# Kernel tuning notes

Hardware: AMD Instinct MI355X
Metric: run time of the kernel (lower is better)

## Reference

```python
import jax, jax.numpy as jnp
import numpy as np

B, T, D, H, L = 8, 150, 30, 5, 3
HD = D // H  # 6
ORIG = (300, 74, 35)


def setup_inputs() -> dict:
    key = jax.random.key(0)
    ks = iter(jax.random.split(key, 40))
    def g(shape, s=0.05):
        return jax.random.normal(next(ks), shape, dtype=jnp.float32) * s
    return {
        "x_l": g((B, T, ORIG[0]), 1.0),
        "x_a": g((B, T, ORIG[1]), 1.0),
        "x_v": g((B, T, ORIG[2]), 1.0),
        "Wl": g((D, ORIG[0])),
        "Wa": g((D, ORIG[1])),
        "Wv": g((D, ORIG[2])),
        "in_w": g((2, L, 3 * D, D)),
        "in_b": jnp.zeros((2, L, 3 * D), jnp.float32),
        "out_w": g((2, L, D, D)),
        "out_b": jnp.zeros((2, L, D), jnp.float32),
        "lin1_w": g((2, L, 4 * D, D)),
        "lin1_b": jnp.zeros((2, L, 4 * D), jnp.float32),
        "lin2_w": g((2, L, D, 4 * D)),
        "lin2_b": jnp.zeros((2, L, D), jnp.float32),
        "n1_g": jnp.ones((2, L, D), jnp.float32),
        "n1_b": jnp.zeros((2, L, D), jnp.float32),
        "n2_g": jnp.ones((2, L, D), jnp.float32),
        "n2_b": jnp.zeros((2, L, D), jnp.float32),
        "p1_w": g((2 * D, 2 * D)),
        "p1_b": jnp.zeros((2 * D,), jnp.float32),
        "p2_w": g((2 * D, 2 * D)),
        "p2_b": jnp.zeros((2 * D,), jnp.float32),
        "ow": g((1, 2 * D)),
        "ob": jnp.zeros((1,), jnp.float32),
    }


def _ln(x, g, b, eps=1e-5):
    m = x.mean(-1, keepdims=True)
    v = jnp.var(x, axis=-1, keepdims=True)  # biased var, matches torch LayerNorm
    return (x - m) * jax.lax.rsqrt(v + eps) * g + b


def _heads(x):  # [Tt, B, D] -> [B*H, Tt, HD]
    Tt = x.shape[0]
    return x.reshape(Tt, B * H, HD).transpose(1, 0, 2)


def _layer(x, xk, xv, p):
    iw, ib, ow, ob, w1, b1, w2, b2, g1, bb1, g2, bb2 = p
    res = x
    xn, kn, vn = _ln(x, g1, bb1), _ln(xk, g1, bb1), _ln(xv, g1, bb1)
    q = (xn @ iw[:D].T + ib[:D]) * (HD ** -0.5)
    k = kn @ iw[D:2 * D].T + ib[D:2 * D]
    v = vn @ iw[2 * D:].T + ib[2 * D:]
    qh, kh, vh = _heads(q), _heads(k), _heads(v)
    # trilinear scores: [B*H, Tq, Tk, Tv]
    aw = jnp.einsum('iat,ibt,ict->iabc', qh, kh, vh)
    fused = aw.mean(-1) + aw.max(-1)          # fuse over value axis -> [B*H, Tq, Tk]
    fused = jax.nn.softmax(fused, axis=-1)
    attn = jnp.einsum('iab,ibt->iat', fused, qh)  # NB: original bmm uses q, not v
    attn = attn.transpose(1, 0, 2).reshape(-1, B, D)
    x = res + (attn @ ow.T + ob)
    res = x
    xn = _ln(x, g2, bb2)
    x = jax.nn.relu(xn @ w1.T + b1) @ w2.T + b2
    return res + x


def reference(x_l, x_a, x_v, Wl, Wa, Wv, in_w, in_b, out_w, out_b,
              lin1_w, lin1_b, lin2_w, lin2_b, n1_g, n1_b, n2_g, n2_b,
              p1_w, p1_b, p2_w, p2_b, ow, ob):
    pl = (x_l @ Wl.T).transpose(1, 0, 2)  # [T, B, D] (conv1d k=1, no bias)
    pa = (x_a @ Wa.T).transpose(1, 0, 2)
    pv = (x_v @ Wv.T).transpose(1, 0, 2)
    hs = []
    for s, (kk, vv) in enumerate(((pa, pv), (pv, pa))):
        h = pl
        for l in range(L):
            p = (in_w[s, l], in_b[s, l], out_w[s, l], out_b[s, l],
                 lin1_w[s, l], lin1_b[s, l], lin2_w[s, l], lin2_b[s, l],
                 n1_g[s, l], n1_b[s, l], n2_g[s, l], n2_b[s, l])
            h = _layer(h, kk, vv, p)
        hs.append(h[-1])  # last timestep [B, D]
    last_hs = jnp.concatenate(hs, axis=1)  # [B, 2D]
    proj = jax.nn.relu(last_hs @ p1_w.T + p1_b) @ p2_w.T + p2_b + last_hs
    out = proj @ ow.T + ob
    return (out, last_hs)
```

## Files before the change

kernel.cpp:

```cpp
#include <hip/hip_runtime.h>
#include <math.h>

#define BB 8
#define TT 150
#define DD 30
#define HH 5
#define HD 6
#define LL 3
#define NI 40
#define ROWF (TT*BB*DD)
#define RSTR 8
#define NR 152

typedef _Float16 half8 __attribute__((ext_vector_type(8)));
typedef float f32x16 __attribute__((ext_vector_type(16)));

__device__ __forceinline__ float wsum(float v) {
    #pragma unroll
    for (int m = 32; m > 0; m >>= 1) v += __shfl_xor(v, m, 64);
    return v;
}

__global__ __launch_bounds__(256) void proj3_kernel(
    const float* __restrict__ x_l, const float* __restrict__ x_a, const float* __restrict__ x_v,
    const float* __restrict__ Wl, const float* __restrict__ Wa, const float* __restrict__ Wv,
    float* __restrict__ pl, float* __restrict__ pa, float* __restrict__ pv) {
    int blk = blockIdx.x;
    int which = blk / 300;
    int w = threadIdx.x >> 6, lane = threadIdx.x & 63;
    int rowu = (blk % 300) * 4 + w;
    int t = rowu / BB, b = rowu % BB;
    const float* x = which == 0 ? x_l : (which == 1 ? x_a : x_v);
    const float* W = which == 0 ? Wl : (which == 1 ? Wa : Wv);
    float* out = which == 0 ? pl : (which == 1 ? pa : pv);
    int Cin = which == 0 ? 300 : (which == 1 ? 74 : 35);
    int cst = Cin + ((Cin & 1) ? 0 : 1);
    __shared__ float WS[30 * 301];
    __shared__ float xr[4][304];
    for (int j = threadIdx.x; j < DD * Cin; j += 256)
        WS[(j / Cin) * cst + (j % Cin)] = W[j];
    const float* xp = x + ((size_t)b * TT + t) * Cin;
    for (int j = lane; j < Cin; j += 64) xr[w][j] = xp[j];
    __syncthreads();
    int d = lane >> 1, jh = lane & 1;
    int h1 = Cin >> 1;
    int j0 = jh ? h1 : 0, j1 = jh ? Cin : h1;
    const float* wr = WS + (size_t)(d < DD ? d : 0) * cst;
    float acc = 0.f;
    for (int j = j0; j < j1; j++) acc += xr[w][j] * wr[j];
    acc += __shfl_xor(acc, 1, 64);
    if (jh == 0 && d < DD) out[t * (BB * DD) + b * DD + d] = acc;
}

__global__ __launch_bounds__(256) void kvpre_kernel(
    const float* __restrict__ pa, const float* __restrict__ pv,
    const float* __restrict__ in_w, const float* __restrict__ in_b,
    const float* __restrict__ n1g, const float* __restrict__ n1b,
    float* __restrict__ k_all, float* __restrict__ v_all) {
    int blk = blockIdx.x;
    int po = blk / 300;
    int s = po / LL;
    int w = threadIdx.x >> 6, lane = threadIdx.x & 63;
    int tb = (blk % 300) * 4 + w;
    int t = tb / BB, b = tb % BB;
    const float* xk = (s == 0) ? pa : pv;
    const float* xv = (s == 0) ? pv : pa;
    const float* iw = in_w + (size_t)po * 2700 + 900;
    const float* ib = in_b + (size_t)po * 90;
    const float* g  = n1g + (size_t)po * 30;
    const float* bb = n1b + (size_t)po * 30;
    __shared__ float iwS[1800];
    __shared__ float xn[4][2][30];
    for (int j = threadIdx.x; j < 1800; j += 256) iwS[j] = iw[j];
    const float* rows[2] = { xk + (size_t)tb * 30, xv + (size_t)tb * 30 };
    for (int r = 0; r < 2; r++) {
        float xval = (lane < 30) ? rows[r][lane] : 0.f;
        float mean = wsum(xval) * (1.f / 30.f);
        float dv = (lane < 30) ? (xval - mean) : 0.f;
        float var = wsum(dv * dv) * (1.f / 30.f);
        float inv = rsqrtf(var + 1e-5f);
        if (lane < 30) xn[w][r][lane] = dv * inv * g[lane] + bb[lane];
    }
    __syncthreads();
    int o = lane;
    if (o < 60) {
        int which = o / 30, dd = o % 30;
        const float* wr = iwS + o * 30;
        const float* xr = xn[w][which];
        float acc = 0.f;
        #pragma unroll 6
        for (int j = 0; j < 30; j++) acc += wr[j] * xr[j];
        acc += ib[30 + o];
        int i = b * HH + dd / HD, hd = dd % HD;
        float* dst = which ? v_all : k_all;
        dst[((size_t)po * NI + i) * (TT * HD) + t * HD + hd] = acc;
    }
}

__global__ __launch_bounds__(256) void lnq0_kernel(
    const float* __restrict__ pl,
    const float* __restrict__ in_w, const float* __restrict__ in_b,
    const float* __restrict__ n1g, const float* __restrict__ n1b,
    float* __restrict__ q) {
    int blk = blockIdx.x;
    int s = blk / 300;
    int w = threadIdx.x >> 6, lane = threadIdx.x & 63;
    int tb = (blk % 300) * 4 + w;
    int t = tb / BB, b = tb % BB;
    int po = s * LL;
    const float* iw = in_w + (size_t)po * 2700;
    const float* ib = in_b + (size_t)po * 90;
    const float* g  = n1g + (size_t)po * 30;
    const float* bb = n1b + (size_t)po * 30;
    __shared__ float iwS[900];
    __shared__ float xn[4][30];
    for (int j = threadIdx.x; j < 900; j += 256) iwS[j] = iw[j];
    const float* row = pl + (size_t)tb * 30;
    float xval = (lane < 30) ? row[lane] : 0.f;
    float mean = wsum(xval) * (1.f / 30.f);
    float dv = (lane < 30) ? (xval - mean) : 0.f;
    float var = wsum(dv * dv) * (1.f / 30.f);
    float inv = rsqrtf(var + 1e-5f);
    if (lane < 30) xn[w][lane] = dv * inv * g[lane] + bb[lane];
    __syncthreads();
    int o = lane;
    if (o < 30) {
        const float* wr = iwS + o * 30;
        float acc = 0.f;
        #pragma unroll 6
        for (int j = 0; j < 30; j++) acc += wr[j] * xn[w][j];
        acc = (acc + ib[o]) * 0.40824829046386307f;
        int i = b * HH + o / HD, hd = o % HD;
        q[((size_t)s * NI + i) * (TT * HD) + t * HD + hd] = acc;
    }
}

__global__ __launch_bounds__(256) void score_kernel(
    const float* __restrict__ q, const float* __restrict__ k_all,
    const float* __restrict__ v_all, int l, float* __restrict__ attn) {
    int blk = blockIdx.x;
    int s = blk / 760;
    int rem = blk % 760;
    int i = rem / 19;
    int g = rem % 19;
    int tid = threadIdx.x;
    int wv = tid >> 6, lane = tid & 63;
    int lo = lane & 31, hf = lane >> 5;
    int po = s * LL + l;

    __shared__ __align__(16) _Float16 qsh[NR * RSTR];
    __shared__ __align__(16) _Float16 ksh[NR * RSTR];
    __shared__ __align__(16) _Float16 vsh[NR * RSTR];

    int* qz = (int*)qsh; int* kz = (int*)ksh; int* vz = (int*)vsh;
    for (int idx = tid; idx < NR * RSTR / 2; idx += 256) {
        qz[idx] = 0; kz[idx] = 0; vz[idx] = 0;
    }
    __syncthreads();
    const float* qg = q + (size_t)(s * NI + i) * (TT * HD);
    const float* kg = k_all + (size_t)(po * NI + i) * (TT * HD);
    const float* vg = v_all + (size_t)(po * NI + i) * (TT * HD);
    for (int idx = tid; idx < TT * HD; idx += 256) {
        int dst = (idx / HD) * RSTR + (idx % HD);
        qsh[dst] = (_Float16)qg[idx];
        ksh[dst] = (_Float16)kg[idx];
        vsh[dst] = (_Float16)vg[idx];
    }
    __syncthreads();
    if (wv == 0) {
        float v6[6] = {0.f, 0.f, 0.f, 0.f, 0.f, 0.f};
        for (int c = lane; c < TT; c += 64) {
            #pragma unroll
            for (int t = 0; t < 6; t++) v6[t] += (float)vsh[c * RSTR + t];
        }
        #pragma unroll
        for (int m = 32; m > 0; m >>= 1) {
            #pragma unroll
            for (int t = 0; t < 6; t++) v6[t] += __shfl_xor(v6[t], m, 64);
        }
        if (lane < 6) vsh[TT * RSTR + lane] = (_Float16)(v6[lane] * (1.f / TT));
    }
    __syncthreads();

    f32x16 zacc;
    #pragma unroll
    for (int j = 0; j < 16; j++) zacc[j] = 0.f;
    half8 zero8;
    #pragma unroll
    for (int t = 0; t < 8; t++) zero8[t] = (_Float16)0.f;

    half8 bfrag[5], vhalf[5];
    #pragma unroll
    for (int nt = 0; nt < 5; nt++) {
        int rr = nt * 32 + lo;
        int rc = rr < 151 ? rr : 151;
        half8 kf = *(const half8*)&ksh[rc * RSTR];
        half8 vf = *(const half8*)&vsh[rc * RSTR];
        bfrag[nt] = hf ? zero8 : kf;
        vhalf[nt] = hf ? zero8 : vf;
    }

    for (int ap = 0; ap < 2; ap++) {
        int a = g * 8 + wv * 2 + ap;
        if (a >= TT) break;
        half8 qav = *(const half8*)&qsh[a * RSTR];
        half8 afrag[5];
        #pragma unroll
        for (int nt = 0; nt < 5; nt++) afrag[nt] = vhalf[nt] * qav;

        float fsc[5];
        #pragma unroll
        for (int nb = 0; nb < 5; nb++) {
            float rm = -INFINITY;
            #pragma unroll
            for (int ma = 0; ma < 4; ma++) {
                f32x16 acc = __builtin_amdgcn_mfma_f32_32x32x16_f16(afrag[ma], bfrag[nb], zacc, 0, 0, 0);
                float m = fmaxf(acc[0], acc[1]);
                #pragma unroll
                for (int j = 2; j < 16; j += 2) m = fmaxf(fmaxf(m, acc[j]), acc[j + 1]);
                rm = fmaxf(rm, m);
            }
            f32x16 a4 = __builtin_amdgcn_mfma_f32_32x32x16_f16(afrag[4], bfrag[nb], zacc, 0, 0, 0);
            float m4 = fmaxf(a4[0], a4[1]);
            #pragma unroll
            for (int j = 2; j < 10; j += 2) m4 = fmaxf(fmaxf(m4, a4[j]), a4[j + 1]);
            float ext = (hf == 0) ? fmaxf(a4[10], a4[11]) : -INFINITY;
            rm = fmaxf(rm, fmaxf(m4, ext));
            float om = __shfl_xor(a4[10], 32, 64);
            float mn = hf ? a4[10] : om;
            rm = fmaxf(rm, __shfl_xor(rm, 32, 64));
            int bcol = nb * 32 + lo;
            fsc[nb] = (bcol < TT) ? (mn + rm) : -INFINITY;
        }
        float m = fsc[0];
        #pragma unroll
        for (int nb = 1; nb < 5; nb++) m = fmaxf(m, fsc[nb]);
        #pragma unroll
        for (int msk = 16; msk > 0; msk >>= 1) m = fmaxf(m, __shfl_xor(m, msk, 64));
        float e[5], es = 0.f;
        #pragma unroll
        for (int nb = 0; nb < 5; nb++) { e[nb] = __expf(fsc[nb] - m); es += e[nb]; }
        #pragma unroll
        for (int msk = 16; msk > 0; msk >>= 1) es += __shfl_xor(es, msk, 64);
        float acc6[6] = {0.f, 0.f, 0.f, 0.f, 0.f, 0.f};
        #pragma unroll
        for (int nb = 0; nb < 5; nb++) {
            int bcol = nb * 32 + lo;
            int bi = (bcol < TT) ? bcol : 0;
            float wgt = e[nb];
            half8 qrow = *(const half8*)&qsh[bi * RSTR];
            #pragma unroll
            for (int t = 0; t < 6; t++) acc6[t] += wgt * (float)qrow[t];
        }
        #pragma unroll
        for (int msk = 16; msk > 0; msk >>= 1) {
            #pragma unroll
            for (int t = 0; t < 6; t++) acc6[t] += __shfl_xor(acc6[t], msk, 64);
        }
        if (lane == 0) {
            float inv = 1.f / es;
            int bo = i / HH, ho = i % HH;
            float* dst = attn + (size_t)s * ROWF + a * (BB * DD) + bo * DD + ho * HD;
            #pragma unroll
            for (int t = 0; t < 6; t++) dst[t] = acc6[t] * inv;
        }
    }
}

__global__ __launch_bounds__(256) void ffnlnq_kernel(
    const float* __restrict__ attn, const float* __restrict__ pl,
    const float* __restrict__ out_w, const float* __restrict__ out_b,
    const float* __restrict__ l1w, const float* __restrict__ l1b,
    const float* __restrict__ l2w, const float* __restrict__ l2b,
    const float* __restrict__ n2g, const float* __restrict__ n2b,
    const float* __restrict__ in_w, const float* __restrict__ in_b,
    const float* __restrict__ n1g, const float* __restrict__ n1b,
    int l, int has_next,
    float* __restrict__ h, float* __restrict__ q) {
    int blk = blockIdx.x;
    int s = blk / 300;
    int w = threadIdx.x >> 6, lane = threadIdx.x & 63;
    int tb = (blk % 300) * 4 + w;
    int t = tb / BB, b = tb % BB;
    int po = s * LL + l;
    const float* ow = out_w + (size_t)po * 900;
    const float* ob = out_b + (size_t)po * 30;
    const float* w1 = l1w + (size_t)po * 3600;
    const float* b1 = l1b + (size_t)po * 120;
    const float* w2 = l2w + (size_t)po * 3600;
    const float* b2 = l2b + (size_t)po * 30;
    const float* g2 = n2g + (size_t)po * 30;
    const float* bb2 = n2b + (size_t)po * 30;
    __shared__ float owS[900];
    __shared__ float w1T[30 * 128];
    __shared__ float w2S[30 * 121];
    __shared__ float iwqS[900];
    __shared__ float arS[4][30], xnS[4][32], hidS[4][120], xqS[4][30];
    for (int j = threadIdx.x; j < 900; j += 256) owS[j] = ow[j];
    for (int j = threadIdx.x; j < 3600; j += 256) w1T[(j % 30) * 128 + (j / 30)] = w1[j];
    for (int j = threadIdx.x; j < 3600; j += 256) w2S[(j / 120) * 121 + (j % 120)] = w2[j];
    if (has_next) {
        const float* iwq = in_w + (size_t)(po + 1) * 2700;
        for (int j = threadIdx.x; j < 900; j += 256) iwqS[j] = iwq[j];
    }
    __syncthreads();
    float* hrow = h + (size_t)s * ROWF + (size_t)tb * 30;
    const float* res = (l == 0) ? (pl + (size_t)tb * 30) : hrow;
    const float* arow = attn + (size_t)s * ROWF + (size_t)tb * 30;
    if (lane < 30) arS[w][lane] = arow[lane];
    float x1v = 0.f;
    if (lane < 30) {
        const float* wr = owS + lane * 30;
        float acc = 0.f;
        #pragma unroll 6
        for (int j = 0; j < 30; j++) acc += wr[j] * arS[w][j];
        x1v = res[lane] + acc + ob[lane];
    }
    float mean = wsum(x1v) * (1.f / 30.f);
    float dv = (lane < 30) ? (x1v - mean) : 0.f;
    float var = wsum(dv * dv) * (1.f / 30.f);
    float inv = rsqrtf(var + 1e-5f);
    if (lane < 30) xnS[w][lane] = dv * inv * g2[lane] + bb2[lane];
    for (int o = lane; o < 120; o += 64) {
        float acc = 0.f;
        #pragma unroll 6
        for (int j = 0; j < 30; j++) acc += w1T[j * 128 + o] * xnS[w][j];
        hidS[w][o] = fmaxf(acc + b1[o], 0.f);
    }
    float newh = 0.f;
    if (lane < 30) {
        const float* wr = w2S + lane * 121;
        float acc = 0.f;
        #pragma unroll 8
        for (int j = 0; j < 120; j++) acc += wr[j] * hidS[w][j];
        newh = x1v + acc + b2[lane];
        hrow[lane] = newh;
    }
    if (has_next) {
        const float* g1 = n1g + (size_t)(po + 1) * 30;
        const float* bb1 = n1b + (size_t)(po + 1) * 30;
        const float* ibq = in_b + (size_t)(po + 1) * 90;
        float mean2 = wsum(newh) * (1.f / 30.f);
        float dv2 = (lane < 30) ? (newh - mean2) : 0.f;
        float var2 = wsum(dv2 * dv2) * (1.f / 30.f);
        float inv2 = rsqrtf(var2 + 1e-5f);
        if (lane < 30) xqS[w][lane] = dv2 * inv2 * g1[lane] + bb1[lane];
        int o = lane;
        if (o < 30) {
            const float* wr = iwqS + o * 30;
            float acc = 0.f;
            #pragma unroll 6
            for (int j = 0; j < 30; j++) acc += wr[j] * xqS[w][j];
            acc = (acc + ibq[o]) * 0.40824829046386307f;
            int i = b * HH + o / HD, hd = o % HD;
            q[((size_t)s * NI + i) * (TT * HD) + t * HD + hd] = acc;
        }
    }
}

__global__ __launch_bounds__(256) void head_kernel(
    const float* __restrict__ h,
    const float* __restrict__ p1w, const float* __restrict__ p1b,
    const float* __restrict__ p2w, const float* __restrict__ p2b,
    const float* __restrict__ ow, const float* __restrict__ ob,
    float* __restrict__ out) {
    int tid = threadIdx.x;
    __shared__ float lh[480], hid[480], pr[480];
    for (int idx = tid; idx < 480; idx += 256) {
        int b = idx / 60, j = idx % 60;
        int s = j / 30, d = j % 30;
        float vv = h[(size_t)s * ROWF + 149 * (BB * DD) + b * DD + d];
        lh[idx] = vv;
        out[8 + idx] = vv;
    }
    __syncthreads();
    for (int idx = tid; idx < 480; idx += 256) {
        int b = idx / 60, o = idx % 60;
        const float* wr = p1w + o * 60;
        float acc = p1b[o];
        for (int j = 0; j < 60; j++) acc += wr[j] * lh[b * 60 + j];
        hid[idx] = fmaxf(acc, 0.f);
    }
    __syncthreads();
    for (int idx = tid; idx < 480; idx += 256) {
        int b = idx / 60, d = idx % 60;
        const float* wr = p2w + d * 60;
        float acc = p2b[d];
        for (int j = 0; j < 60; j++) acc += wr[j] * hid[b * 60 + j];
        pr[idx] = acc + lh[idx];
    }
    __syncthreads();
    if (tid < 8) {
        float acc = ob[0];
        for (int j = 0; j < 60; j++) acc += pr[tid * 60 + j] * ow[j];
        out[tid] = acc;
    }
}

extern "C" void kernel_launch(void* const* d_in, const int* in_sizes, int n_in,
                              void* d_out, int out_size, void* d_ws, size_t ws_size,
                              hipStream_t stream) {
    const float* x_l   = (const float*)d_in[0];
    const float* x_a   = (const float*)d_in[1];
    const float* x_v   = (const float*)d_in[2];
    const float* Wl    = (const float*)d_in[3];
    const float* Wa    = (const float*)d_in[4];
    const float* Wv    = (const float*)d_in[5];
    const float* in_w  = (const float*)d_in[6];
    const float* in_b  = (const float*)d_in[7];
    const float* out_w = (const float*)d_in[8];
    const float* out_b = (const float*)d_in[9];
    const float* l1w   = (const float*)d_in[10];
    const float* l1b   = (const float*)d_in[11];
    const float* l2w   = (const float*)d_in[12];
    const float* l2b   = (const float*)d_in[13];
    const float* n1g   = (const float*)d_in[14];
    const float* n1b   = (const float*)d_in[15];
    const float* n2g   = (const float*)d_in[16];
    const float* n2b   = (const float*)d_in[17];
    const float* p1w   = (const float*)d_in[18];
    const float* p1b   = (const float*)d_in[19];
    const float* p2w   = (const float*)d_in[20];
    const float* p2b   = (const float*)d_in[21];
    const float* oww   = (const float*)d_in[22];
    const float* obb   = (const float*)d_in[23];

    float* ws = (float*)d_ws;
    float* pl    = ws;
    float* pa    = ws + 36000;
    float* pv    = ws + 72000;
    float* h     = ws + 108000;
    float* q     = ws + 180000;
    float* k_all = ws + 252000;
    float* v_all = ws + 468000;
    float* at    = ws + 684000;

    proj3_kernel<<<900, 256, 0, stream>>>(x_l, x_a, x_v, Wl, Wa, Wv, pl, pa, pv);
    kvpre_kernel<<<1800, 256, 0, stream>>>(pa, pv, in_w, in_b, n1g, n1b, k_all, v_all);
    lnq0_kernel<<<600, 256, 0, stream>>>(pl, in_w, in_b, n1g, n1b, q);

    for (int l = 0; l < LL; l++) {
        score_kernel<<<1520, 256, 0, stream>>>(q, k_all, v_all, l, at);
        ffnlnq_kernel<<<600, 256, 0, stream>>>(at, pl, out_w, out_b, l1w, l1b, l2w, l2b,
                                               n2g, n2b, in_w, in_b, n1g, n1b,
                                               l, (l < LL - 1) ? 1 : 0, h, q);
    }
    head_kernel<<<1, 256, 0, stream>>>(h, p1w, p1b, p2w, p2b, oww, obb, (float*)d_out);
}
```

Before: 254.2 us.

## Fuse all stages into one cooperative persistent kernel with grid syncs

Replaces the ten separate kernel launches with a single cooperative persistent kernel. Blocks loop over tasks for each stage and use grid.sync between stages, which removes launch gaps and per-launch overhead. The input-projection weights are now staged in shared memory as fp16. The grid is capped at 768 blocks with two blocks per CU, so each block handles several tasks per stage serially and grid-wide barriers are added. The old multi-kernel path stays as a fallback.

```diff
diff --git a/kernel.cpp b/kernel.cpp
--- a/kernel.cpp
+++ b/kernel.cpp
@@ -1,5 +1,8 @@
 #include <hip/hip_runtime.h>
+#include <hip/hip_cooperative_groups.h>
 #include <math.h>
+
+namespace cg = cooperative_groups;
 
 #define BB 8
 #define TT 150
@@ -11,14 +14,390 @@
 #define ROWF (TT*BB*DD)
 #define RSTR 8
 #define NR 152
+#define SMEMN 9904
 
 typedef _Float16 half8 __attribute__((ext_vector_type(8)));
 typedef float f32x16 __attribute__((ext_vector_type(16)));
+
+struct Params {
+    const float *x_l, *x_a, *x_v, *Wl, *Wa, *Wv;
+    const float *in_w, *in_b, *out_w, *out_b;
+    const float *l1w, *l1b, *l2w, *l2b;
+    const float *n1g, *n1b, *n2g, *n2b;
+    const float *p1w, *p1b, *p2w, *p2b, *oww, *obb;
+    float *pl, *pa, *pv, *h, *q, *k_all, *v_all, *at, *out;
+};
 
 __device__ __forceinline__ float wsum(float v) {
     #pragma unroll
     for (int m = 32; m > 0; m >>= 1) v += __shfl_xor(v, m, 64);
     return v;
+}
+
+__global__ __launch_bounds__(256, 2) void mega_kernel(Params P) {
+    cg::grid_group grid = cg::this_grid();
+    __shared__ __align__(16) float sm[SMEMN];
+    const int tid = threadIdx.x;
+    const int w = tid >> 6, lane = tid & 63;
+    const int nbk = gridDim.x, bid = blockIdx.x;
+
+    {
+        _Float16* WH = (_Float16*)sm;
+        float* xr = sm + 4520;
+        for (int task = bid; task < 900; task += nbk) {
+            int which = task / 300;
+            int rowu = (task % 300) * 4 + w;
+            int t = rowu / BB, b = rowu % BB;
+            const float* x = which == 0 ? P.x_l : (which == 1 ? P.x_a : P.x_v);
+            const float* W = which == 0 ? P.Wl : (which == 1 ? P.Wa : P.Wv);
+            float* outp = which == 0 ? P.pl : (which == 1 ? P.pa : P.pv);
+            int Cin = which == 0 ? 300 : (which == 1 ? 74 : 35);
+            int cst = Cin | 1;
+            for (int j = tid; j < DD * Cin; j += 256)
+                WH[(j / Cin) * cst + (j % Cin)] = (_Float16)W[j];
+            const float* xp = x + ((size_t)b * TT + t) * Cin;
+            for (int j = lane; j < Cin; j += 64) xr[w * 304 + j] = xp[j];
+            __syncthreads();
+            int d = lane >> 1, jh = lane & 1;
+            int h1 = Cin >> 1;
+            int j0 = jh ? h1 : 0, j1 = jh ? Cin : h1;
+            const _Float16* wr = WH + (d < DD ? d : 0) * cst;
+            float acc = 0.f;
+            for (int j = j0; j < j1; j++) acc += xr[w * 304 + j] * (float)wr[j];
+            acc += __shfl_xor(acc, 1, 64);
+            if (jh == 0 && d < DD) outp[t * (BB * DD) + b * DD + d] = acc;
+            __syncthreads();
+        }
+    }
+    __threadfence();
+    grid.sync();
+
+    {
+        float* iwS = sm;
+        float* xn  = sm + 1800;
+        for (int task = bid; task < 1800; task += nbk) {
+            int po = task / 300;
+            int s = po / LL;
+            int tb = (task % 300) * 4 + w;
+            int t = tb / BB, b = tb % BB;
+            const float* xk = (s == 0) ? P.pa : P.pv;
+            const float* xv = (s == 0) ? P.pv : P.pa;
+            const float* iw = P.in_w + (size_t)po * 2700 + 900;
+            const float* ib = P.in_b + (size_t)po * 90;
+            const float* g  = P.n1g + (size_t)po * 30;
+            const float* bb = P.n1b + (size_t)po * 30;
+            for (int j = tid; j < 1800; j += 256) iwS[j] = iw[j];
+            const float* rows[2] = { xk + (size_t)tb * 30, xv + (size_t)tb * 30 };
+            for (int r = 0; r < 2; r++) {
+                float xval = (lane < 30) ? rows[r][lane] : 0.f;
+                float mean = wsum(xval) * (1.f / 30.f);
+                float dv = (lane < 30) ? (xval - mean) : 0.f;
+                float var = wsum(dv * dv) * (1.f / 30.f);
+                float inv = rsqrtf(var + 1e-5f);
+                if (lane < 30) xn[w * 60 + r * 30 + lane] = dv * inv * g[lane] + bb[lane];
+            }
+            __syncthreads();
+            if (lane < 60) {
+                int which = lane / 30, dd = lane % 30;
+                const float* wr = iwS + lane * 30;
+                const float* xv2 = xn + w * 60 + which * 30;
+                float acc = 0.f;
+                #pragma unroll 6
+                for (int j = 0; j < 30; j++) acc += wr[j] * xv2[j];
+                acc += ib[30 + lane];
+                int i = b * HH + dd / HD, hd = dd % HD;
+                float* dst = which ? P.v_all : P.k_all;
+                dst[((size_t)po * NI + i) * (TT * HD) + t * HD + hd] = acc;
+            }
+            __syncthreads();
+        }
+        float* iwq = sm;
+        float* xn2 = sm + 900;
+        for (int task = bid; task < 600; task += nbk) {
+            int s = task / 300;
+            int tb = (task % 300) * 4 + w;
+            int t = tb / BB, b = tb % BB;
+            int po = s * LL;
+            const float* iw = P.in_w + (size_t)po * 2700;
+            const float* ib = P.in_b + (size_t)po * 90;
+            const float* g  = P.n1g + (size_t)po * 30;
+            const float* bb = P.n1b + (size_t)po * 30;
+            for (int j = tid; j < 900; j += 256) iwq[j] = iw[j];
+            const float* row = P.pl + (size_t)tb * 30;
+            float xval = (lane < 30) ? row[lane] : 0.f;
+            float mean = wsum(xval) * (1.f / 30.f);
+            float dv = (lane < 30) ? (xval - mean) : 0.f;
+            float var = wsum(dv * dv) * (1.f / 30.f);
+            float inv = rsqrtf(var + 1e-5f);
+            if (lane < 30) xn2[w * 30 + lane] = dv * inv * g[lane] + bb[lane];
+            __syncthreads();
+            if (lane < 30) {
+                const float* wr = iwq + lane * 30;
+                float acc = 0.f;
+                #pragma unroll 6
+                for (int j = 0; j < 30; j++) acc += wr[j] * xn2[w * 30 + j];
+                acc = (acc + ib[lane]) * 0.40824829046386307f;
+                int i = b * HH + lane / HD, hd = lane % HD;
+                P.q[((size_t)s * NI + i) * (TT * HD) + t * HD + hd] = acc;
+            }
+            __syncthreads();
+        }
+    }
+    __threadfence();
+    grid.sync();
+
+    for (int l = 0; l < LL; l++) {
+        {
+            _Float16* qsh = (_Float16*)sm;
+            _Float16* ksh = qsh + NR * RSTR;
+            _Float16* vsh = ksh + NR * RSTR;
+            const int lo = lane & 31, hf = lane >> 5;
+            for (int task = bid; task < 1520; task += nbk) {
+                int s = task / 760;
+                int rem = task % 760;
+                int i = rem / 19;
+                int g = rem % 19;
+                int po = s * LL + l;
+                int* z = (int*)sm;
+                for (int idx = tid; idx < 3 * NR * RSTR / 2; idx += 256) z[idx] = 0;
+                __syncthreads();
+                const float* qg = P.q + (size_t)(s * NI + i) * (TT * HD);
+                const float* kg = P.k_all + (size_t)(po * NI + i) * (TT * HD);
+                const float* vg = P.v_all + (size_t)(po * NI + i) * (TT * HD);
+                for (int idx = tid; idx < TT * HD; idx += 256) {
+                    int dst = (idx / HD) * RSTR + (idx % HD);
+                    qsh[dst] = (_Float16)qg[idx];
+                    ksh[dst] = (_Float16)kg[idx];
+                    vsh[dst] = (_Float16)vg[idx];
+                }
+                __syncthreads();
+                if (w == 0) {
+                    float v6[6] = {0.f, 0.f, 0.f, 0.f, 0.f, 0.f};
+                    for (int c = lane; c < TT; c += 64) {
+                        #pragma unroll
+                        for (int t = 0; t < 6; t++) v6[t] += (float)vsh[c * RSTR + t];
+                    }
+                    #pragma unroll
+                    for (int m = 32; m > 0; m >>= 1) {
+                        #pragma unroll
+                        for (int t = 0; t < 6; t++) v6[t] += __shfl_xor(v6[t], m, 64);
+                    }
+                    if (lane < 6) vsh[TT * RSTR + lane] = (_Float16)(v6[lane] * (1.f / TT));
+                }
+                __syncthreads();
+
+                f32x16 zacc;
+                #pragma unroll
+                for (int j = 0; j < 16; j++) zacc[j] = 0.f;
+                half8 zero8;
+                #pragma unroll
+                for (int t = 0; t < 8; t++) zero8[t] = (_Float16)0.f;
+
+                half8 bfrag[5], vhalf[5];
+                #pragma unroll
+                for (int nt = 0; nt < 5; nt++) {
+                    int rr = nt * 32 + lo;
+                    int rc = rr < 151 ? rr : 151;
+                    half8 kf = *(const half8*)&ksh[rc * RSTR];
+                    half8 vf = *(const half8*)&vsh[rc * RSTR];
+                    bfrag[nt] = hf ? zero8 : kf;
+                    vhalf[nt] = hf ? zero8 : vf;
+                }
+
+                for (int ap = 0; ap < 2; ap++) {
+                    int a = g * 8 + w * 2 + ap;
+                    if (a >= TT) break;
+                    half8 qav = *(const half8*)&qsh[a * RSTR];
+                    half8 afrag[5];
+                    #pragma unroll
+                    for (int nt = 0; nt < 5; nt++) afrag[nt] = vhalf[nt] * qav;
+
+                    float fsc[5];
+                    #pragma unroll
+                    for (int nb = 0; nb < 5; nb++) {
+                        float rm = -INFINITY;
+                        #pragma unroll
+                        for (int ma = 0; ma < 4; ma++) {
+                            f32x16 acc = __builtin_amdgcn_mfma_f32_32x32x16_f16(afrag[ma], bfrag[nb], zacc, 0, 0, 0);
+                            float m = fmaxf(acc[0], acc[1]);
+                            #pragma unroll
+                            for (int j = 2; j < 16; j += 2) m = fmaxf(fmaxf(m, acc[j]), acc[j + 1]);
+                            rm = fmaxf(rm, m);
+                        }
+                        f32x16 a4 = __builtin_amdgcn_mfma_f32_32x32x16_f16(afrag[4], bfrag[nb], zacc, 0, 0, 0);
+                        float m4 = fmaxf(a4[0], a4[1]);
+                        #pragma unroll
+                        for (int j = 2; j < 10; j += 2) m4 = fmaxf(fmaxf(m4, a4[j]), a4[j + 1]);
+                        float ext = (hf == 0) ? fmaxf(a4[10], a4[11]) : -INFINITY;
+                        rm = fmaxf(rm, fmaxf(m4, ext));
+                        float om = __shfl_xor(a4[10], 32, 64);
+                        float mn = hf ? a4[10] : om;
+                        rm = fmaxf(rm, __shfl_xor(rm, 32, 64));
+                        int bcol = nb * 32 + lo;
+                        fsc[nb] = (bcol < TT) ? (mn + rm) : -INFINITY;
+                    }
+                    float m = fsc[0];
+                    #pragma unroll
+                    for (int nb = 1; nb < 5; nb++) m = fmaxf(m, fsc[nb]);
+                    #pragma unroll
+                    for (int msk = 16; msk > 0; msk >>= 1) m = fmaxf(m, __shfl_xor(m, msk, 64));
+                    float e[5], es = 0.f;
+                    #pragma unroll
+                    for (int nb = 0; nb < 5; nb++) { e[nb] = __expf(fsc[nb] - m); es += e[nb]; }
+                    #pragma unroll
+                    for (int msk = 16; msk > 0; msk >>= 1) es += __shfl_xor(es, msk, 64);
+                    float acc6[6] = {0.f, 0.f, 0.f, 0.f, 0.f, 0.f};
+                    #pragma unroll
+                    for (int nb = 0; nb < 5; nb++) {
+                        int bcol = nb * 32 + lo;
+                        int bi = (bcol < TT) ? bcol : 0;
+                        float wgt = e[nb];
+                        half8 qrow = *(const half8*)&qsh[bi * RSTR];
+                        #pragma unroll
+                        for (int t = 0; t < 6; t++) acc6[t] += wgt * (float)qrow[t];
+                    }
+                    #pragma unroll
+                    for (int msk = 16; msk > 0; msk >>= 1) {
+                        #pragma unroll
+                        for (int t = 0; t < 6; t++) acc6[t] += __shfl_xor(acc6[t], msk, 64);
+                    }
+                    if (lane == 0) {
+                        float inv = 1.f / es;
+                        int bo = i / HH, ho = i % HH;
+                        float* dst = P.at + (size_t)s * ROWF + a * (BB * DD) + bo * DD + ho * HD;
+                        #pragma unroll
+                        for (int t = 0; t < 6; t++) dst[t] = acc6[t] * inv;
+                    }
+                }
+                __syncthreads();
+            }
+        }
+        __threadfence();
+        grid.sync();
+
+        {
+            float* owS  = sm;
+            float* w1T  = sm + 900;
+            float* w2S  = sm + 4500;
+            float* iwqS = sm + 8130;
+            float* arS  = sm + 9030;
+            float* xnS  = sm + 9150;
+            float* hidS = sm + 9278;
+            float* xqS  = sm + 9758;
+            int has_next = (l < LL - 1);
+            for (int task = bid; task < 600; task += nbk) {
+                int s = task / 300;
+                int tb = (task % 300) * 4 + w;
+                int t = tb / BB, b = tb % BB;
+                int po = s * LL + l;
+                const float* ow = P.out_w + (size_t)po * 900;
+                const float* ob = P.out_b + (size_t)po * 30;
+                const float* w1 = P.l1w + (size_t)po * 3600;
+                const float* b1 = P.l1b + (size_t)po * 120;
+                const float* w2 = P.l2w + (size_t)po * 3600;
+                const float* b2 = P.l2b + (size_t)po * 30;
+                const float* g2 = P.n2g + (size_t)po * 30;
+                const float* bb2 = P.n2b + (size_t)po * 30;
+                for (int j = tid; j < 900; j += 256) owS[j] = ow[j];
+                for (int j = tid; j < 3600; j += 256) w1T[(j % 30) * 120 + (j / 30)] = w1[j];
+                for (int j = tid; j < 3600; j += 256) w2S[(j / 120) * 121 + (j % 120)] = w2[j];
+                if (has_next) {
+                    const float* iwq = P.in_w + (size_t)(po + 1) * 2700;
+                    for (int j = tid; j < 900; j += 256) iwqS[j] = iwq[j];
+                }
+                float* hrow = P.h + (size_t)s * ROWF + (size_t)tb * 30;
+                const float* res = (l == 0) ? (P.pl + (size_t)tb * 30) : hrow;
+                const float* arow = P.at + (size_t)s * ROWF + (size_t)tb * 30;
+                if (lane < 30) arS[w * 30 + lane] = arow[lane];
+                __syncthreads();
+                float x1v = 0.f;
+                if (lane < 30) {
+                    const float* wr = owS + lane * 30;
+                    float acc = 0.f;
+                    #pragma unroll 6
+                    for (int j = 0; j < 30; j++) acc += wr[j] * arS[w * 30 + j];
+                    x1v = res[lane] + acc + ob[lane];
+                }
+                float mean = wsum(x1v) * (1.f / 30.f);
+                float dv = (lane < 30) ? (x1v - mean) : 0.f;
+                float var = wsum(dv * dv) * (1.f / 30.f);
+                float inv = rsqrtf(var + 1e-5f);
+                if (lane < 30) xnS[w * 32 + lane] = dv * inv * g2[lane] + bb2[lane];
+                for (int o = lane; o < 120; o += 64) {
+                    float acc = 0.f;
+                    #pragma unroll 6
+                    for (int j = 0; j < 30; j++) acc += w1T[j * 120 + o] * xnS[w * 32 + j];
+                    hidS[w * 120 + o] = fmaxf(acc + b1[o], 0.f);
+                }
+                float newh = 0.f;
+                if (lane < 30) {
+                    const float* wr = w2S + lane * 121;
+                    float acc = 0.f;
+                    #pragma unroll 8
+                    for (int j = 0; j < 120; j++) acc += wr[j] * hidS[w * 120 + j];
+                    newh = x1v + acc + b2[lane];
+                    hrow[lane] = newh;
+                }
+                if (has_next) {
+                    const float* g1 = P.n1g + (size_t)(po + 1) * 30;
+                    const float* bb1 = P.n1b + (size_t)(po + 1) * 30;
+                    const float* ibq = P.in_b + (size_t)(po + 1) * 90;
+                    float mean2 = wsum(newh) * (1.f / 30.f);
+                    float dv2 = (lane < 30) ? (newh - mean2) : 0.f;
+                    float var2 = wsum(dv2 * dv2) * (1.f / 30.f);
+                    float inv2 = rsqrtf(var2 + 1e-5f);
+                    if (lane < 30) xqS[w * 30 + lane] = dv2 * inv2 * g1[lane] + bb1[lane];
+                    if (lane < 30) {
+                        const float* wr = iwqS + lane * 30;
+                        float acc = 0.f;
+                        #pragma unroll 6
+                        for (int j = 0; j < 30; j++) acc += wr[j] * xqS[w * 30 + j];
+                        acc = (acc + ibq[lane]) * 0.40824829046386307f;
+                        int i = b * HH + lane / HD, hd = lane % HD;
+                        P.q[((size_t)s * NI + i) * (TT * HD) + t * HD + hd] = acc;
+                    }
+                }
+                __syncthreads();
+            }
+        }
+        __threadfence();
+        grid.sync();
+    }
+
+    if (bid == 0) {
+        float* lh  = sm;
+        float* hid = sm + 480;
+        float* pr  = sm + 960;
+        for (int idx = tid; idx < 480; idx += 256) {
+            int b = idx / 60, j = idx % 60;
+            int s = j / 30, d = j % 30;
+            float vv = P.h[(size_t)s * ROWF + 149 * (BB * DD) + b * DD + d];
+            lh[idx] = vv;
+            P.out[8 + idx] = vv;
+        }
+        __syncthreads();
+        for (int idx = tid; idx < 480; idx += 256) {
+            int b = idx / 60, o = idx % 60;
+            const float* wr = P.p1w + o * 60;
+            float acc = P.p1b[o];
+            for (int j = 0; j < 60; j++) acc += wr[j] * lh[b * 60 + j];
+            hid[idx] = fmaxf(acc, 0.f);
+        }
+        __syncthreads();
+        for (int idx = tid; idx < 480; idx += 256) {
+            int b = idx / 60, d = idx % 60;
+            const float* wr = P.p2w + d * 60;
+            float acc = P.p2b[d];
+            for (int j = 0; j < 60; j++) acc += wr[j] * hid[b * 60 + j];
+            pr[idx] = acc + lh[idx];
+        }
+        __syncthreads();
+        if (tid < 8) {
+            float acc = P.obb[0];
+            for (int j = 0; j < 60; j++) acc += pr[tid * 60 + j] * P.oww[j];
+            P.out[tid] = acc;
+        }
+    }
 }
 
 __global__ __launch_bounds__(256) void proj3_kernel(
@@ -34,7 +413,7 @@
     const float* W = which == 0 ? Wl : (which == 1 ? Wa : Wv);
     float* out = which == 0 ? pl : (which == 1 ? pa : pv);
     int Cin = which == 0 ? 300 : (which == 1 ? 74 : 35);
-    int cst = Cin + ((Cin & 1) ? 0 : 1);
+    int cst = Cin | 1;
     __shared__ float WS[30 * 301];
     __shared__ float xr[4][304];
     for (int j = threadIdx.x; j < DD * Cin; j += 256)
@@ -82,15 +461,14 @@
         if (lane < 30) xn[w][r][lane] = dv * inv * g[lane] + bb[lane];
     }
     __syncthreads();
-    int o = lane;
-    if (o < 60) {
-        int which = o / 30, dd = o % 30;
-        const float* wr = iwS + o * 30;
-        const float* xr = xn[w][which];
+    if (lane < 60) {
+        int which = lane / 30, dd = lane % 30;
+        const float* wr = iwS + lane * 30;
+        const float* xv2 = xn[w][which];
         float acc = 0.f;
         #pragma unroll 6
-        for (int j = 0; j < 30; j++) acc += wr[j] * xr[j];
-        acc += ib[30 + o];
+        for (int j = 0; j < 30; j++) acc += wr[j] * xv2[j];
+        acc += ib[30 + lane];
         int i = b * HH + dd / HD, hd = dd % HD;
         float* dst = which ? v_all : k_all;
         dst[((size_t)po * NI + i) * (TT * HD) + t * HD + hd] = acc;
@@ -123,14 +501,13 @@
     float inv = rsqrtf(var + 1e-5f);
     if (lane < 30) xn[w][lane] = dv * inv * g[lane] + bb[lane];
     __syncthreads();
-    int o = lane;
-    if (o < 30) {
-        const float* wr = iwS + o * 30;
+    if (lane < 30) {
+        const float* wr = iwS + lane * 30;
         float acc = 0.f;
         #pragma unroll 6
         for (int j = 0; j < 30; j++) acc += wr[j] * xn[w][j];
-        acc = (acc + ib[o]) * 0.40824829046386307f;
-        int i = b * HH + o / HD, hd = o % HD;
+        acc = (acc + ib[lane]) * 0.40824829046386307f;
+        int i = b * HH + lane / HD, hd = lane % HD;
         q[((size_t)s * NI + i) * (TT * HD) + t * HD + hd] = acc;
     }
 }
@@ -147,15 +524,11 @@
     int wv = tid >> 6, lane = tid & 63;
     int lo = lane & 31, hf = lane >> 5;
     int po = s * LL + l;
-
     __shared__ __align__(16) _Float16 qsh[NR * RSTR];
     __shared__ __align__(16) _Float16 ksh[NR * RSTR];
     __shared__ __align__(16) _Float16 vsh[NR * RSTR];
-
     int* qz = (int*)qsh; int* kz = (int*)ksh; int* vz = (int*)vsh;
-    for (int idx = tid; idx < NR * RSTR / 2; idx += 256) {
-        qz[idx] = 0; kz[idx] = 0; vz[idx] = 0;
-    }
+    for (int idx = tid; idx < NR * RSTR / 2; idx += 256) { qz[idx] = 0; kz[idx] = 0; vz[idx] = 0; }
     __syncthreads();
     const float* qg = q + (size_t)(s * NI + i) * (TT * HD);
     const float* kg = k_all + (size_t)(po * NI + i) * (TT * HD);
@@ -181,14 +554,12 @@
         if (lane < 6) vsh[TT * RSTR + lane] = (_Float16)(v6[lane] * (1.f / TT));
     }
     __syncthreads();
-
     f32x16 zacc;
     #pragma unroll
     for (int j = 0; j < 16; j++) zacc[j] = 0.f;
     half8 zero8;
     #pragma unroll
     for (int t = 0; t < 8; t++) zero8[t] = (_Float16)0.f;
-
     half8 bfrag[5], vhalf[5];
     #pragma unroll
     for (int nt = 0; nt < 5; nt++) {
@@ -199,7 +570,6 @@
         bfrag[nt] = hf ? zero8 : kf;
         vhalf[nt] = hf ? zero8 : vf;
     }
-
     for (int ap = 0; ap < 2; ap++) {
         int a = g * 8 + wv * 2 + ap;
         if (a >= TT) break;
@@ -207,7 +577,6 @@
         half8 afrag[5];
         #pragma unroll
         for (int nt = 0; nt < 5; nt++) afrag[nt] = vhalf[nt] * qav;
-
         float fsc[5];
         #pragma unroll
         for (int nb = 0; nb < 5; nb++) {
@@ -308,6 +677,7 @@
     const float* res = (l == 0) ? (pl + (size_t)tb * 30) : hrow;
     const float* arow = attn + (size_t)s * ROWF + (size_t)tb * 30;
     if (lane < 30) arS[w][lane] = arow[lane];
+    __syncthreads();
     float x1v = 0.f;
     if (lane < 30) {
         const float* wr = owS + lane * 30;
@@ -345,14 +715,13 @@
         float var2 = wsum(dv2 * dv2) * (1.f / 30.f);
         float inv2 = rsqrtf(var2 + 1e-5f);
         if (lane < 30) xqS[w][lane] = dv2 * inv2 * g1[lane] + bb1[lane];
-        int o = lane;
-        if (o < 30) {
-            const float* wr = iwqS + o * 30;
+        if (lane < 30) {
+            const float* wr = iwqS + lane * 30;
             float acc = 0.f;
             #pragma unroll 6
             for (int j = 0; j < 30; j++) acc += wr[j] * xqS[w][j];
-            acc = (acc + ibq[o]) * 0.40824829046386307f;
-            int i = b * HH + o / HD, hd = o % HD;
+            acc = (acc + ibq[lane]) * 0.40824829046386307f;
+            int i = b * HH + lane / HD, hd = lane % HD;
             q[((size_t)s * NI + i) * (TT * HD) + t * HD + hd] = acc;
         }
     }
@@ -400,50 +769,75 @@
 extern "C" void kernel_launch(void* const* d_in, const int* in_sizes, int n_in,
                               void* d_out, int out_size, void* d_ws, size_t ws_size,
                               hipStream_t stream) {
-    const float* x_l   = (const float*)d_in[0];
-    const float* x_a   = (const float*)d_in[1];
-    const float* x_v   = (const float*)d_in[2];
-    const float* Wl    = (const float*)d_in[3];
-    const float* Wa    = (const float*)d_in[4];
-    const float* Wv    = (const float*)d_in[5];
-    const float* in_w  = (const float*)d_in[6];
-    const float* in_b  = (const float*)d_in[7];
-    const float* out_w = (const float*)d_in[8];
-    const float* out_b = (const float*)d_in[9];
-    const float* l1w   = (const float*)d_in[10];
-    const float* l1b   = (const float*)d_in[11];
-    const float* l2w   = (const float*)d_in[12];
-    const float* l2b   = (const float*)d_in[13];
-    const float* n1g   = (const float*)d_in[14];
-    const float* n1b   = (const float*)d_in[15];
-    const float* n2g   = (const float*)d_in[16];
-    const float* n2b   = (const float*)d_in[17];
-    const float* p1w   = (const float*)d_in[18];
-    const float* p1b   = (const float*)d_in[19];
-    const float* p2w   = (const float*)d_in[20];
-    const float* p2b   = (const float*)d_in[21];
-    const float* oww   = (const float*)d_in[22];
-    const float* obb   = (const float*)d_in[23];
-
     float* ws = (float*)d_ws;
-    float* pl    = ws;
-    float* pa    = ws + 36000;
-    float* pv    = ws + 72000;
-    float* h     = ws + 108000;
-    float* q     = ws + 180000;
-    float* k_all = ws + 252000;
-    float* v_all = ws + 468000;
-    float* at    = ws + 684000;
-
-    proj3_kernel<<<900, 256, 0, stream>>>(x_l, x_a, x_v, Wl, Wa, Wv, pl, pa, pv);
-    kvpre_kernel<<<1800, 256, 0, stream>>>(pa, pv, in_w, in_b, n1g, n1b, k_all, v_all);
-    lnq0_kernel<<<600, 256, 0, stream>>>(pl, in_w, in_b, n1g, n1b, q);
-
-    for (int l = 0; l < LL; l++) {
-        score_kernel<<<1520, 256, 0, stream>>>(q, k_all, v_all, l, at);
-        ffnlnq_kernel<<<600, 256, 0, stream>>>(at, pl, out_w, out_b, l1w, l1b, l2w, l2b,
-                                               n2g, n2b, in_w, in_b, n1g, n1b,
-                                               l, (l < LL - 1) ? 1 : 0, h, q);
-    }
-    head_kernel<<<1, 256, 0, stream>>>(h, p1w, p1b, p2w, p2b, oww, obb, (float*)d_out);
+    Params P;
+    P.x_l  = (const float*)d_in[0];
+    P.x_a  = (const float*)d_in[1];
+    P.x_v  = (const float*)d_in[2];
+    P.Wl   = (const float*)d_in[3];
+    P.Wa   = (const float*)d_in[4];
+    P.Wv   = (const float*)d_in[5];
+    P.in_w = (const float*)d_in[6];
+    P.in_b = (const float*)d_in[7];
+    P.out_w = (const float*)d_in[8];
+    P.out_b = (const float*)d_in[9];
+    P.l1w  = (const float*)d_in[10];
+    P.l1b  = (const float*)d_in[11];
+    P.l2w  = (const float*)d_in[12];
+    P.l2b  = (const float*)d_in[13];
+    P.n1g  = (const float*)d_in[14];
+    P.n1b  = (const float*)d_in[15];
+    P.n2g  = (const float*)d_in[16];
+    P.n2b  = (const float*)d_in[17];
+    P.p1w  = (const float*)d_in[18];
+    P.p1b  = (const float*)d_in[19];
+    P.p2w  = (const float*)d_in[20];
+    P.p2b  = (const float*)d_in[21];
+    P.oww  = (const float*)d_in[22];
+    P.obb  = (const float*)d_in[23];
+    P.pl    = ws;
+    P.pa    = ws + 36000;
+    P.pv    = ws + 72000;
+    P.h     = ws + 108000;
+    P.q     = ws + 180000;
+    P.k_all = ws + 252000;
+    P.v_all = ws + 468000;
+    P.at    = ws + 684000;
+    P.out   = (float*)d_out;
+
+    int dev = 0;
+    hipGetDevice(&dev);
+    int coopAttr = 0;
+    hipDeviceGetAttribute(&coopAttr, hipDeviceAttributeCooperativeLaunch, dev);
+    int cus = 0;
+    hipDeviceGetAttribute(&cus, hipDeviceAttributeMultiprocessorCount, dev);
+    int maxBpc = 0;
+    hipOccupancyMaxActiveBlocksPerMultiprocessor(&maxBpc, mega_kernel, 256, 0);
+
+    bool launched = false;
+    if (coopAttr && maxBpc >= 1 && cus >= 1) {
+        int blocks = maxBpc * cus;
+        if (blocks > 768) blocks = 768;
+        void* args[] = { &P };
+        hipError_t e = hipLaunchCooperativeKernel((const void*)mega_kernel,
+                                                  dim3(blocks), dim3(256), args, 0, stream);
+        launched = (e == hipSuccess);
+    }
+    if (!launched) {
+        proj3_kernel<<<900, 256, 0, stream>>>(P.x_l, P.x_a, P.x_v, P.Wl, P.Wa, P.Wv,
+                                              P.pl, P.pa, P.pv);
+        kvpre_kernel<<<1800, 256, 0, stream>>>(P.pa, P.pv, P.in_w, P.in_b, P.n1g, P.n1b,
+                                               P.k_all, P.v_all);
+        lnq0_kernel<<<600, 256, 0, stream>>>(P.pl, P.in_w, P.in_b, P.n1g, P.n1b, P.q);
+        for (int l = 0; l < LL; l++) {
+            score_kernel<<<1520, 256, 0, stream>>>(P.q, P.k_all, P.v_all, l, P.at);
+            ffnlnq_kernel<<<600, 256, 0, stream>>>(P.at, P.pl, P.out_w, P.out_b,
+                                                   P.l1w, P.l1b, P.l2w, P.l2b,
+                                                   P.n2g, P.n2b, P.in_w, P.in_b,
+                                                   P.n1g, P.n1b, l, (l < LL - 1) ? 1 : 0,
+                                                   P.h, P.q);
+        }
+        head_kernel<<<1, 256, 0, stream>>>(P.h, P.p1w, P.p1b, P.p2w, P.p2b,
+                                           P.oww, P.obb, P.out);
+    }
 }
```

Result: slower. 797.6 us (+213.7%).
